# Optimization experiments

Hardware: AMD Instinct MI355X
Metric: run time of the kernel (lower is better)

## Reference

```python
import jax, jax.numpy as jnp
import numpy as np

N, K, D = 65536, 4096, 64


def setup_inputs() -> dict:
    key = jax.random.key(0)
    kx, ke = jax.random.split(key)
    x = jax.random.normal(kx, (N, D), dtype=jnp.float32)
    embed = jax.random.normal(ke, (1, K, D), dtype=jnp.float32)
    return {"x": x, "embed": embed}


def reference(x, embed):
    # Faithful to EuclideanCodebook.forward quantization path:
    #   dist = cdist(flatten, embed, p=2)**2 ; argmin ; one_hot @ embed
    xf = x.astype(jnp.float32)            # [N, D]
    e = embed[0]                          # [K, D]
    # squared euclidean distance via expansion (== cdist(...).pow(2))
    x_sq = jnp.sum(xf * xf, axis=-1, keepdims=True)        # [N, 1]
    e_sq = jnp.sum(e * e, axis=-1)                          # [K]
    dist = jnp.maximum(x_sq + e_sq[None, :] - 2.0 * (xf @ e.T), 0.0)  # [N, K]
    embed_ind = jnp.argmin(dist, axis=-1)                   # [N]
    # one_hot @ embed is exactly a row gather of the codebook
    quantize = e[embed_ind]                                 # [N, D]
    return quantize, embed_ind[None, :]                     # embed_ind kept as [1, N] like torch
```

## Files before the change

kernel.cpp:

```cpp
#include <hip/hip_runtime.h>
#include <math.h>

#define N_ROWS 65536
#define K_CODES 4096
#define NTILES_TOTAL (K_CODES / 32)
#define K_CHUNKS 4
#define NTILES (NTILES_TOTAL / K_CHUNKS)
#define DIM 64
#define NBUF 2
#define ACC_MARGIN 0.005f

typedef __attribute__((ext_vector_type(8))) short bf16x8;
typedef __attribute__((ext_vector_type(4))) float f32x4;

__device__ inline unsigned short f2bf_rne(float f) {
    unsigned u = __float_as_uint(f);
    return (unsigned short)((u + 0x7FFFu + ((u >> 16) & 1u)) >> 16);
}
__device__ inline float bf2f(unsigned short s) {
    return __uint_as_float(((unsigned)s) << 16);
}

__global__ __launch_bounds__(256) void pack_e(const float* __restrict__ embed,
                                              short* __restrict__ e_pk,
                                              float* __restrict__ esq,
                                              float* __restrict__ esqn,
                                              int* __restrict__ count) {
    __shared__ float lds_f[2048];
    const int tile = blockIdx.x;
    const int t = threadIdx.x;
    if (tile == 0 && t == 0) *count = 0;
    const float4* src = (const float4*)(embed + (size_t)tile * 2048);
    ((float4*)lds_f)[t] = src[t];
    ((float4*)lds_f)[t + 256] = src[t + 256];
    __syncthreads();
    const int l = t & 63;
    const int kh = (t >> 6) & 1;
    const int ch = (t >> 7) & 1;
    const int base = (ch * 16 + (l & 15)) * 64 + kh * 32 + ((l >> 4) & 3) * 8;
    bf16x8 vh, vl;
#pragma unroll
    for (int j = 0; j < 8; ++j) {
        float v = lds_f[base + j];
        unsigned short h = f2bf_rne(v);
        vh[j] = (short)h;
        vl[j] = (short)f2bf_rne(v - bf2f(h));
    }
    *(bf16x8*)(e_pk + (size_t)tile * 4096 + t * 8) = vh;
    *(bf16x8*)(e_pk + (size_t)tile * 4096 + 2048 + t * 8) = vl;
    if (t < 32) {
        float s = 0.f;
#pragma unroll
        for (int d = 0; d < 64; ++d) { float v = lds_f[t * 64 + d]; s = fmaf(v, v, s); }
        esq[tile * 32 + t] = s;
        esqn[tile * 32 + t] = -0.5f * s;
    }
}

__global__ __launch_bounds__(256, 4) void vq_main(const float* __restrict__ x,
                                                  const short* __restrict__ e_pk,
                                                  const float* __restrict__ esqn,
                                                  float* __restrict__ b1s,
                                                  float* __restrict__ b2s,
                                                  int* __restrict__ i1s) {
    __shared__ __align__(16) char lds[NBUF][8192];
    __shared__ __align__(16) float lds_q[NBUF][64];
    const int tid = threadIdx.x;
    const int wid = tid >> 6;
    const int l = tid & 63;
    const int c16 = l & 15;
    const int rgrp = (l >> 4) & 3;
    const int kc = blockIdx.x & (K_CHUNKS - 1);
    const int rg = blockIdx.x >> 2;
    const int rowbase = rg * 128 + wid * 32;
    const int tile0 = kc * NTILES;

    bf16x8 ah[2][2], al[2][2];
#pragma unroll
    for (int rh = 0; rh < 2; ++rh) {
        const float* xr = x + (size_t)(rowbase + rh * 16 + c16) * DIM;
#pragma unroll
        for (int kh = 0; kh < 2; ++kh) {
            const float* p = xr + kh * 32 + rgrp * 8;
#pragma unroll
            for (int j = 0; j < 8; ++j) {
                float v = p[j];
                unsigned short h = f2bf_rne(v);
                ah[rh][kh][j] = (short)h;
                al[rh][kh][j] = (short)f2bf_rne(v - bf2f(h));
            }
        }
    }

    float b1[8], b2[8];
    int i1[8];
#pragma unroll
    for (int i = 0; i < 8; ++i) { b1[i] = -3.0e38f; b2[i] = -3.0e38f; i1[i] = 0; }

    auto stage = [&](int t, int b) {
        const char* gsrc = (const char*)e_pk + (size_t)(tile0 + t) * 8192 + tid * 16;
        __builtin_amdgcn_global_load_lds(
            (const __attribute__((address_space(1))) void*)gsrc,
            (__attribute__((address_space(3))) void*)(&lds[b][wid * 1024]), 16, 0, 0);
        __builtin_amdgcn_global_load_lds(
            (const __attribute__((address_space(1))) void*)(gsrc + 4096),
            (__attribute__((address_space(3))) void*)(&lds[b][4096 + wid * 1024]), 16, 0, 0);
        const float* qsrc = esqn + (size_t)(tile0 + t) * 32 + l;
        __builtin_amdgcn_global_load_lds(
            (const __attribute__((address_space(1))) void*)qsrc,
            (__attribute__((address_space(3))) void*)(&lds_q[b][0]), 4, 0, 0);
    };

    stage(0, 0);

    for (int t = 0; t < NTILES; ++t) {
        const int cur = t & 1;
        asm volatile("s_waitcnt vmcnt(0) lgkmcnt(0)" ::: "memory");
        __builtin_amdgcn_sched_barrier(0);
        __builtin_amdgcn_s_barrier();
        __builtin_amdgcn_sched_barrier(0);
        if (t + 1 < NTILES) stage(t + 1, cur ^ 1);

        const float eq0 = lds_q[cur][c16];
        const float eq1 = lds_q[cur][16 + c16];
        const int ci0 = (tile0 + t) * 32 + c16;
        const int ci1 = ci0 + 16;

        bf16x8 bh[2][2], bl[2][2];
#pragma unroll
        for (int ch = 0; ch < 2; ++ch)
#pragma unroll
            for (int kh = 0; kh < 2; ++kh) {
                const int fo = ((ch * 2 + kh) * 64 + l) * 16;
                bh[ch][kh] = *(const bf16x8*)(&lds[cur][fo]);
                bl[ch][kh] = *(const bf16x8*)(&lds[cur][4096 + fo]);
            }

        f32x4 a00 = {eq0, eq0, eq0, eq0};
        f32x4 a01 = {eq1, eq1, eq1, eq1};
        f32x4 a10 = {eq0, eq0, eq0, eq0};
        f32x4 a11 = {eq1, eq1, eq1, eq1};

        __builtin_amdgcn_s_setprio(1);
#pragma unroll
        for (int kh = 0; kh < 2; ++kh) {
            a00 = __builtin_amdgcn_mfma_f32_16x16x32_bf16(ah[0][kh], bh[0][kh], a00, 0, 0, 0);
            a01 = __builtin_amdgcn_mfma_f32_16x16x32_bf16(ah[0][kh], bh[1][kh], a01, 0, 0, 0);
            a10 = __builtin_amdgcn_mfma_f32_16x16x32_bf16(ah[1][kh], bh[0][kh], a10, 0, 0, 0);
            a11 = __builtin_amdgcn_mfma_f32_16x16x32_bf16(ah[1][kh], bh[1][kh], a11, 0, 0, 0);
            a00 = __builtin_amdgcn_mfma_f32_16x16x32_bf16(ah[0][kh], bl[0][kh], a00, 0, 0, 0);
            a01 = __builtin_amdgcn_mfma_f32_16x16x32_bf16(ah[0][kh], bl[1][kh], a01, 0, 0, 0);
            a10 = __builtin_amdgcn_mfma_f32_16x16x32_bf16(ah[1][kh], bl[0][kh], a10, 0, 0, 0);
            a11 = __builtin_amdgcn_mfma_f32_16x16x32_bf16(ah[1][kh], bl[1][kh], a11, 0, 0, 0);
            a00 = __builtin_amdgcn_mfma_f32_16x16x32_bf16(al[0][kh], bh[0][kh], a00, 0, 0, 0);
            a01 = __builtin_amdgcn_mfma_f32_16x16x32_bf16(al[0][kh], bh[1][kh], a01, 0, 0, 0);
            a10 = __builtin_amdgcn_mfma_f32_16x16x32_bf16(al[1][kh], bh[0][kh], a10, 0, 0, 0);
            a11 = __builtin_amdgcn_mfma_f32_16x16x32_bf16(al[1][kh], bh[1][kh], a11, 0, 0, 0);
        }
        __builtin_amdgcn_s_setprio(0);

#define TRACK2(V0, V1, E)                                            \
        {                                                            \
            float v0 = (V0), v1 = (V1);                              \
            bool g0 = v0 > b1[E];                                    \
            b2[E] = __builtin_amdgcn_fmed3f(v0, b1[E], b2[E]);       \
            b1[E] = fmaxf(v0, b1[E]);                                \
            i1[E] = g0 ? ci0 : i1[E];                                \
            bool g1 = v1 > b1[E];                                    \
            b2[E] = __builtin_amdgcn_fmed3f(v1, b1[E], b2[E]);       \
            b1[E] = fmaxf(v1, b1[E]);                                \
            i1[E] = g1 ? ci1 : i1[E];                                \
        }
#pragma unroll
        for (int j = 0; j < 4; ++j) {
            TRACK2(a00[j], a01[j], j)
            TRACK2(a10[j], a11[j], 4 + j)
        }
#undef TRACK2
    }

#pragma unroll
    for (int e = 0; e < 8; ++e) {
#pragma unroll
        for (int m = 1; m <= 8; m <<= 1) {
            float ob1 = __shfl_xor(b1[e], m);
            float ob2 = __shfl_xor(b2[e], m);
            int oi = __shfl_xor(i1[e], m);
            float nb2 = fmaxf(fminf(b1[e], ob1), fmaxf(b2[e], ob2));
            bool take = ob1 > b1[e];
            b1[e] = take ? ob1 : b1[e];
            i1[e] = take ? oi : i1[e];
            b2[e] = nb2;
        }
        if (c16 == 0) {
            int row = rowbase + (e >> 2) * 16 + rgrp * 4 + (e & 3);
            b1s[(size_t)kc * N_ROWS + row] = b1[e];
            b2s[(size_t)kc * N_ROWS + row] = b2[e];
            i1s[(size_t)kc * N_ROWS + row] = i1[e];
        }
    }
}

__global__ __launch_bounds__(256) void vq_merge_gather(const float* __restrict__ embed,
                                                       const float* __restrict__ b1s,
                                                       const float* __restrict__ b2s,
                                                       const int* __restrict__ i1s,
                                                       float* __restrict__ out_q,
                                                       float* __restrict__ out_ind,
                                                       int* __restrict__ list,
                                                       int* __restrict__ count) {
    int t = blockIdx.x * 256 + threadIdx.x;
    int r = t >> 3, q = t & 7;
    float m1 = b1s[r];
    float m2 = b2s[r];
    int idx = i1s[r];
#pragma unroll
    for (int c = 1; c < K_CHUNKS; ++c) {
        float c1 = b1s[(size_t)c * N_ROWS + r];
        float c2 = b2s[(size_t)c * N_ROWS + r];
        int ci = i1s[(size_t)c * N_ROWS + r];
        bool take = c1 > m1;
        m2 = fmaxf(fminf(m1, c1), fmaxf(m2, c2));
        m1 = fmaxf(m1, c1);
        idx = take ? ci : idx;
    }
    const float4* src = (const float4*)(embed + (size_t)idx * DIM + q * 8);
    float4* dst = (float4*)(out_q + (size_t)r * DIM + q * 8);
    dst[0] = src[0];
    dst[1] = src[1];
    if (q == 0) {
        out_ind[r] = (float)idx;
        if (m1 - m2 < ACC_MARGIN) {
            int p = atomicAdd(count, 1);
            list[p] = r;
        }
    }
}

__global__ __launch_bounds__(256) void vq_rescore(const float* __restrict__ x,
                                                  const float* __restrict__ embed,
                                                  const float* __restrict__ esq,
                                                  const int* __restrict__ list,
                                                  const int* __restrict__ count,
                                                  float* __restrict__ out_q,
                                                  float* __restrict__ out_ind) {
    __shared__ float xs[64];
    __shared__ float sk[256];
    __shared__ int si[256];
    const int tid = threadIdx.x;
    const int n = *count;
    for (int f = blockIdx.x; f < n; f += gridDim.x) {
        const int row = list[f];
        if (tid < 16) ((float4*)xs)[tid] = ((const float4*)(x + (size_t)row * DIM))[tid];
        __syncthreads();
        float best = 3.0e38f;
        int bi = 0;
        for (int i = 0; i < 16; ++i) {
            int c = tid + (i << 8);
            const float* e = embed + (size_t)c * DIM;
            float d0 = 0, d1 = 0, d2 = 0, d3 = 0;
#pragma unroll
            for (int d = 0; d < 64; d += 4) {
                d0 = fmaf(xs[d + 0], e[d + 0], d0);
                d1 = fmaf(xs[d + 1], e[d + 1], d1);
                d2 = fmaf(xs[d + 2], e[d + 2], d2);
                d3 = fmaf(xs[d + 3], e[d + 3], d3);
            }
            float key = fmaf(-2.f, (d0 + d1) + (d2 + d3), esq[c]);
            if (key < best) { best = key; bi = c; }
        }
        sk[tid] = best; si[tid] = bi;
        __syncthreads();
        for (int s = 128; s > 0; s >>= 1) {
            if (tid < s) {
                float ok = sk[tid + s]; int oi = si[tid + s];
                if (ok < sk[tid] || (ok == sk[tid] && oi < si[tid])) { sk[tid] = ok; si[tid] = oi; }
            }
            __syncthreads();
        }
        if (tid == 0) out_ind[row] = (float)si[0];
        if (tid < 16) {
            const float4* src = (const float4*)(embed + (size_t)si[0] * DIM);
            ((float4*)(out_q + (size_t)row * DIM))[tid] = src[tid];
        }
        __syncthreads();
    }
}

extern "C" void kernel_launch(void* const* d_in, const int* in_sizes, int n_in,
                              void* d_out, int out_size, void* d_ws, size_t ws_size,
                              hipStream_t stream) {
    const float* x = (const float*)d_in[0];
    const float* embed = (const float*)d_in[1];
    float* out = (float*)d_out;
    float* out_ind = out + (size_t)N_ROWS * DIM;

    char* ws = (char*)d_ws;
    short* e_pk = (short*)ws;
    size_t off = 1 << 20;
    float* esq = (float*)(ws + off);  off += 17 << 10;
    float* esqn = (float*)(ws + off); off += 17 << 10;
    float* b1s = (float*)(ws + off);  off += (size_t)K_CHUNKS * N_ROWS * 4;
    float* b2s = (float*)(ws + off);  off += (size_t)K_CHUNKS * N_ROWS * 4;
    int* i1s = (int*)(ws + off);      off += (size_t)K_CHUNKS * N_ROWS * 4;
    int* list = (int*)(ws + off);     off += (size_t)N_ROWS * 4;
    int* count = (int*)(ws + off);

    pack_e<<<NTILES_TOTAL, 256, 0, stream>>>(embed, e_pk, esq, esqn, count);
    vq_main<<<(N_ROWS / 128) * K_CHUNKS, 256, 0, stream>>>(x, e_pk, esqn, b1s, b2s, i1s);
    vq_merge_gather<<<N_ROWS * 8 / 256, 256, 0, stream>>>(embed, b1s, b2s, i1s,
                                                          out, out_ind, list, count);
    vq_rescore<<<512, 256, 0, stream>>>(x, embed, esq, list, count, out, out_ind);
}
```

Before: 149.7 us.

## Software-pipeline MFMA tiles with deferred argmin tracking across two accumulator sets

Unrolls the tile loop by two and keeps two sets of accumulators, so the argmin/top-2 tracking for one tile is issued after the MFMAs for the next tile, overlapping VALU compare work with matrix-core latency. B fragments are now loaded from LDS inside the kh loop rather than all up front. Launch bounds drop from 4 to 2 waves-per-EU minimum to allow the extra accumulator registers, which may reduce occupancy.

Result: no change. 151.5 us (+1.2%).

```diff
diff --git a/kernel.cpp b/kernel.cpp
--- a/kernel.cpp
+++ b/kernel.cpp
@@ -57,7 +57,7 @@
     }
 }
 
-__global__ __launch_bounds__(256, 4) void vq_main(const float* __restrict__ x,
+__global__ __launch_bounds__(256, 2) void vq_main(const float* __restrict__ x,
                                                   const short* __restrict__ e_pk,
                                                   const float* __restrict__ esqn,
                                                   float* __restrict__ b1s,
@@ -113,71 +113,90 @@
 
     stage(0, 0);
 
-    for (int t = 0; t < NTILES; ++t) {
-        const int cur = t & 1;
-        asm volatile("s_waitcnt vmcnt(0) lgkmcnt(0)" ::: "memory");
-        __builtin_amdgcn_sched_barrier(0);
-        __builtin_amdgcn_s_barrier();
-        __builtin_amdgcn_sched_barrier(0);
-        if (t + 1 < NTILES) stage(t + 1, cur ^ 1);
-
-        const float eq0 = lds_q[cur][c16];
-        const float eq1 = lds_q[cur][16 + c16];
-        const int ci0 = (tile0 + t) * 32 + c16;
-        const int ci1 = ci0 + 16;
-
-        bf16x8 bh[2][2], bl[2][2];
-#pragma unroll
-        for (int ch = 0; ch < 2; ++ch)
-#pragma unroll
-            for (int kh = 0; kh < 2; ++kh) {
-                const int fo = ((ch * 2 + kh) * 64 + l) * 16;
-                bh[ch][kh] = *(const bf16x8*)(&lds[cur][fo]);
-                bl[ch][kh] = *(const bf16x8*)(&lds[cur][4096 + fo]);
-            }
-
-        f32x4 a00 = {eq0, eq0, eq0, eq0};
-        f32x4 a01 = {eq1, eq1, eq1, eq1};
-        f32x4 a10 = {eq0, eq0, eq0, eq0};
-        f32x4 a11 = {eq1, eq1, eq1, eq1};
-
-        __builtin_amdgcn_s_setprio(1);
-#pragma unroll
-        for (int kh = 0; kh < 2; ++kh) {
-            a00 = __builtin_amdgcn_mfma_f32_16x16x32_bf16(ah[0][kh], bh[0][kh], a00, 0, 0, 0);
-            a01 = __builtin_amdgcn_mfma_f32_16x16x32_bf16(ah[0][kh], bh[1][kh], a01, 0, 0, 0);
-            a10 = __builtin_amdgcn_mfma_f32_16x16x32_bf16(ah[1][kh], bh[0][kh], a10, 0, 0, 0);
-            a11 = __builtin_amdgcn_mfma_f32_16x16x32_bf16(ah[1][kh], bh[1][kh], a11, 0, 0, 0);
-            a00 = __builtin_amdgcn_mfma_f32_16x16x32_bf16(ah[0][kh], bl[0][kh], a00, 0, 0, 0);
-            a01 = __builtin_amdgcn_mfma_f32_16x16x32_bf16(ah[0][kh], bl[1][kh], a01, 0, 0, 0);
-            a10 = __builtin_amdgcn_mfma_f32_16x16x32_bf16(ah[1][kh], bl[0][kh], a10, 0, 0, 0);
-            a11 = __builtin_amdgcn_mfma_f32_16x16x32_bf16(ah[1][kh], bl[1][kh], a11, 0, 0, 0);
-            a00 = __builtin_amdgcn_mfma_f32_16x16x32_bf16(al[0][kh], bh[0][kh], a00, 0, 0, 0);
-            a01 = __builtin_amdgcn_mfma_f32_16x16x32_bf16(al[0][kh], bh[1][kh], a01, 0, 0, 0);
-            a10 = __builtin_amdgcn_mfma_f32_16x16x32_bf16(al[1][kh], bh[0][kh], a10, 0, 0, 0);
-            a11 = __builtin_amdgcn_mfma_f32_16x16x32_bf16(al[1][kh], bh[1][kh], a11, 0, 0, 0);
-        }
-        __builtin_amdgcn_s_setprio(0);
-
-#define TRACK2(V0, V1, E)                                            \
+    f32x4 aA00, aA01, aA10, aA11;
+    f32x4 aB00, aB01, aB10, aB11;
+    int pci0 = 0;
+
+#define BARRIER_STAGE(T, CUR)                                          \
+    asm volatile("s_waitcnt vmcnt(0) lgkmcnt(0)" ::: "memory");        \
+    __builtin_amdgcn_sched_barrier(0);                                 \
+    __builtin_amdgcn_s_barrier();                                      \
+    __builtin_amdgcn_sched_barrier(0);                                 \
+    if ((T) + 1 < NTILES) stage((T) + 1, (CUR) ^ 1);
+
+#define MFMA_TILE(CUR, A00, A01, A10, A11)                             \
+    {                                                                  \
+        const float eq0 = lds_q[CUR][c16];                             \
+        const float eq1 = lds_q[CUR][16 + c16];                        \
+        A00 = (f32x4){eq0, eq0, eq0, eq0};                             \
+        A01 = (f32x4){eq1, eq1, eq1, eq1};                             \
+        A10 = (f32x4){eq0, eq0, eq0, eq0};                             \
+        A11 = (f32x4){eq1, eq1, eq1, eq1};                             \
+        __builtin_amdgcn_s_setprio(1);                                 \
+        _Pragma("unroll")                                              \
+        for (int kh = 0; kh < 2; ++kh) {                               \
+            const int fo0 = ((0 * 2 + kh) * 64 + l) * 16;              \
+            const int fo1 = ((1 * 2 + kh) * 64 + l) * 16;              \
+            const bf16x8 bh0 = *(const bf16x8*)(&lds[CUR][fo0]);       \
+            const bf16x8 bh1 = *(const bf16x8*)(&lds[CUR][fo1]);       \
+            const bf16x8 bl0 = *(const bf16x8*)(&lds[CUR][4096 + fo0]); \
+            const bf16x8 bl1 = *(const bf16x8*)(&lds[CUR][4096 + fo1]); \
+            A00 = __builtin_amdgcn_mfma_f32_16x16x32_bf16(ah[0][kh], bh0, A00, 0, 0, 0); \
+            A01 = __builtin_amdgcn_mfma_f32_16x16x32_bf16(ah[0][kh], bh1, A01, 0, 0, 0); \
+            A10 = __builtin_amdgcn_mfma_f32_16x16x32_bf16(ah[1][kh], bh0, A10, 0, 0, 0); \
+            A11 = __builtin_amdgcn_mfma_f32_16x16x32_bf16(ah[1][kh], bh1, A11, 0, 0, 0); \
+            A00 = __builtin_amdgcn_mfma_f32_16x16x32_bf16(ah[0][kh], bl0, A00, 0, 0, 0); \
+            A01 = __builtin_amdgcn_mfma_f32_16x16x32_bf16(ah[0][kh], bl1, A01, 0, 0, 0); \
+            A10 = __builtin_amdgcn_mfma_f32_16x16x32_bf16(ah[1][kh], bl0, A10, 0, 0, 0); \
+            A11 = __builtin_amdgcn_mfma_f32_16x16x32_bf16(ah[1][kh], bl1, A11, 0, 0, 0); \
+            A00 = __builtin_amdgcn_mfma_f32_16x16x32_bf16(al[0][kh], bh0, A00, 0, 0, 0); \
+            A01 = __builtin_amdgcn_mfma_f32_16x16x32_bf16(al[0][kh], bh1, A01, 0, 0, 0); \
+            A10 = __builtin_amdgcn_mfma_f32_16x16x32_bf16(al[1][kh], bh0, A10, 0, 0, 0); \
+            A11 = __builtin_amdgcn_mfma_f32_16x16x32_bf16(al[1][kh], bh1, A11, 0, 0, 0); \
+        }                                                              \
+        __builtin_amdgcn_s_setprio(0);                                 \
+    }
+
+#define TRACK2(V0, V1, E, CI0, CI1)                                  \
         {                                                            \
             float v0 = (V0), v1 = (V1);                              \
             bool g0 = v0 > b1[E];                                    \
             b2[E] = __builtin_amdgcn_fmed3f(v0, b1[E], b2[E]);       \
             b1[E] = fmaxf(v0, b1[E]);                                \
-            i1[E] = g0 ? ci0 : i1[E];                                \
+            i1[E] = g0 ? (CI0) : i1[E];                              \
             bool g1 = v1 > b1[E];                                    \
             b2[E] = __builtin_amdgcn_fmed3f(v1, b1[E], b2[E]);       \
             b1[E] = fmaxf(v1, b1[E]);                                \
-            i1[E] = g1 ? ci1 : i1[E];                                \
-        }
-#pragma unroll
-        for (int j = 0; j < 4; ++j) {
-            TRACK2(a00[j], a01[j], j)
-            TRACK2(a10[j], a11[j], 4 + j)
-        }
+            i1[E] = g1 ? (CI1) : i1[E];                              \
+        }
+
+#define TRACK_SET(A00, A01, A10, A11, CI0)                             \
+    {                                                                  \
+        const int tci0 = (CI0);                                        \
+        const int tci1 = tci0 + 16;                                    \
+        _Pragma("unroll")                                              \
+        for (int j = 0; j < 4; ++j) {                                  \
+            TRACK2(A00[j], A01[j], j, tci0, tci1)                      \
+            TRACK2(A10[j], A11[j], 4 + j, tci0, tci1)                  \
+        }                                                              \
+    }
+
+#pragma unroll 1
+    for (int t = 0; t < NTILES; t += 2) {
+        BARRIER_STAGE(t, 0);
+        MFMA_TILE(0, aA00, aA01, aA10, aA11);
+        if (t > 0) TRACK_SET(aB00, aB01, aB10, aB11, pci0);
+        BARRIER_STAGE(t + 1, 1);
+        MFMA_TILE(1, aB00, aB01, aB10, aB11);
+        TRACK_SET(aA00, aA01, aA10, aA11, (tile0 + t) * 32 + c16);
+        pci0 = (tile0 + t + 1) * 32 + c16;
+    }
+    TRACK_SET(aB00, aB01, aB10, aB11, pci0);
+
+#undef TRACK_SET
 #undef TRACK2
-    }
+#undef MFMA_TILE
+#undef BARRIER_STAGE
 
 #pragma unroll
     for (int e = 0; e < 8; ++e) {
```

## Drop low-bf16 x term in MFMA scoring and batch rescore over rows

Applied to the files above, without the earlier changes.

The main distance kernel stops splitting x into high and low bf16 parts, which removes a third of the MFMA work per tile. The near-tie margin is widened so that more rows fall back to exact fp32 rescoring, which offsets the lost precision. The rescore kernel now handles 8 rows per block and reuses each codebook load across them, and it launches with a larger grid. The risk is that the candidate list grows much longer, so rescore cost could eat the savings, and correctness depends on the margin covering the bf16 error.

Measured after the change: 430.5 us. 188% more time.

```diff
diff --git a/kernel.cpp b/kernel.cpp
--- a/kernel.cpp
+++ b/kernel.cpp
@@ -8,7 +8,8 @@
 #define NTILES (NTILES_TOTAL / K_CHUNKS)
 #define DIM 64
 #define NBUF 2
-#define ACC_MARGIN 0.005f
+#define ACC_MARGIN 0.15f
+#define RR 8
 
 typedef __attribute__((ext_vector_type(8))) short bf16x8;
 typedef __attribute__((ext_vector_type(4))) float f32x4;
@@ -75,7 +76,7 @@
     const int rowbase = rg * 128 + wid * 32;
     const int tile0 = kc * NTILES;
 
-    bf16x8 ah[2][2], al[2][2];
+    bf16x8 ah[2][2];
 #pragma unroll
     for (int rh = 0; rh < 2; ++rh) {
         const float* xr = x + (size_t)(rowbase + rh * 16 + c16) * DIM;
@@ -83,12 +84,8 @@
         for (int kh = 0; kh < 2; ++kh) {
             const float* p = xr + kh * 32 + rgrp * 8;
 #pragma unroll
-            for (int j = 0; j < 8; ++j) {
-                float v = p[j];
-                unsigned short h = f2bf_rne(v);
-                ah[rh][kh][j] = (short)h;
-                al[rh][kh][j] = (short)f2bf_rne(v - bf2f(h));
-            }
+            for (int j = 0; j < 8; ++j)
+                ah[rh][kh][j] = (short)f2bf_rne(p[j]);
         }
     }
 
@@ -152,10 +149,6 @@
             a01 = __builtin_amdgcn_mfma_f32_16x16x32_bf16(ah[0][kh], bl[1][kh], a01, 0, 0, 0);
             a10 = __builtin_amdgcn_mfma_f32_16x16x32_bf16(ah[1][kh], bl[0][kh], a10, 0, 0, 0);
             a11 = __builtin_amdgcn_mfma_f32_16x16x32_bf16(ah[1][kh], bl[1][kh], a11, 0, 0, 0);
-            a00 = __builtin_amdgcn_mfma_f32_16x16x32_bf16(al[0][kh], bh[0][kh], a00, 0, 0, 0);
-            a01 = __builtin_amdgcn_mfma_f32_16x16x32_bf16(al[0][kh], bh[1][kh], a01, 0, 0, 0);
-            a10 = __builtin_amdgcn_mfma_f32_16x16x32_bf16(al[1][kh], bh[0][kh], a10, 0, 0, 0);
-            a11 = __builtin_amdgcn_mfma_f32_16x16x32_bf16(al[1][kh], bh[1][kh], a11, 0, 0, 0);
         }
         __builtin_amdgcn_s_setprio(0);
 
@@ -244,46 +237,72 @@
                                                   const int* __restrict__ count,
                                                   float* __restrict__ out_q,
                                                   float* __restrict__ out_ind) {
-    __shared__ float xs[64];
+    __shared__ float xs[RR][64];
+    __shared__ int rowids[RR];
     __shared__ float sk[256];
     __shared__ int si[256];
     const int tid = threadIdx.x;
     const int n = *count;
-    for (int f = blockIdx.x; f < n; f += gridDim.x) {
-        const int row = list[f];
-        if (tid < 16) ((float4*)xs)[tid] = ((const float4*)(x + (size_t)row * DIM))[tid];
+    for (int base = blockIdx.x * RR; base < n; base += gridDim.x * RR) {
+        const int nr = min(RR, n - base);
         __syncthreads();
-        float best = 3.0e38f;
-        int bi = 0;
+        if (tid < nr) rowids[tid] = list[base + tid];
+        __syncthreads();
+        if (tid < nr * 16) {
+            int r = tid >> 4, q = tid & 15;
+            ((float4*)xs[r])[q] = ((const float4*)(x + (size_t)rowids[r] * DIM))[q];
+        }
+        __syncthreads();
+
+        float best[RR];
+        int bi[RR];
+#pragma unroll
+        for (int r = 0; r < RR; ++r) { best[r] = 3.0e38f; bi[r] = 0; }
+
         for (int i = 0; i < 16; ++i) {
-            int c = tid + (i << 8);
-            const float* e = embed + (size_t)c * DIM;
-            float d0 = 0, d1 = 0, d2 = 0, d3 = 0;
-#pragma unroll
-            for (int d = 0; d < 64; d += 4) {
-                d0 = fmaf(xs[d + 0], e[d + 0], d0);
-                d1 = fmaf(xs[d + 1], e[d + 1], d1);
-                d2 = fmaf(xs[d + 2], e[d + 2], d2);
-                d3 = fmaf(xs[d + 3], e[d + 3], d3);
-            }
-            float key = fmaf(-2.f, (d0 + d1) + (d2 + d3), esq[c]);
-            if (key < best) { best = key; bi = c; }
-        }
-        sk[tid] = best; si[tid] = bi;
-        __syncthreads();
-        for (int s = 128; s > 0; s >>= 1) {
-            if (tid < s) {
-                float ok = sk[tid + s]; int oi = si[tid + s];
-                if (ok < sk[tid] || (ok == sk[tid] && oi < si[tid])) { sk[tid] = ok; si[tid] = oi; }
-            }
+            const int c = tid + (i << 8);
+            const float4* e4 = (const float4*)(embed + (size_t)c * DIM);
+            float dot[RR];
+#pragma unroll
+            for (int r = 0; r < RR; ++r) dot[r] = 0.f;
+#pragma unroll
+            for (int q = 0; q < 16; ++q) {
+                float4 ev = e4[q];
+#pragma unroll
+                for (int r = 0; r < RR; ++r) {
+                    float4 xv = ((const float4*)xs[r])[q];
+                    dot[r] = fmaf(xv.x, ev.x, dot[r]);
+                    dot[r] = fmaf(xv.y, ev.y, dot[r]);
+                    dot[r] = fmaf(xv.z, ev.z, dot[r]);
+                    dot[r] = fmaf(xv.w, ev.w, dot[r]);
+                }
+            }
+            const float eq = esq[c];
+#pragma unroll
+            for (int r = 0; r < RR; ++r) {
+                float key = fmaf(-2.f, dot[r], eq);
+                if (key < best[r]) { best[r] = key; bi[r] = c; }
+            }
+        }
+
+        for (int r = 0; r < nr; ++r) {
+            sk[tid] = best[r];
+            si[tid] = bi[r];
             __syncthreads();
-        }
-        if (tid == 0) out_ind[row] = (float)si[0];
-        if (tid < 16) {
-            const float4* src = (const float4*)(embed + (size_t)si[0] * DIM);
-            ((float4*)(out_q + (size_t)row * DIM))[tid] = src[tid];
-        }
-        __syncthreads();
+            for (int s = 128; s > 0; s >>= 1) {
+                if (tid < s) {
+                    float ok = sk[tid + s]; int oi = si[tid + s];
+                    if (ok < sk[tid] || (ok == sk[tid] && oi < si[tid])) { sk[tid] = ok; si[tid] = oi; }
+                }
+                __syncthreads();
+            }
+            if (tid == 0) out_ind[rowids[r]] = (float)si[0];
+            if (tid < 16) {
+                ((float4*)(out_q + (size_t)rowids[r] * DIM))[tid] =
+                    ((const float4*)(embed + (size_t)si[0] * DIM))[tid];
+            }
+            __syncthreads();
+        }
     }
 }
 
@@ -310,5 +329,5 @@
     vq_main<<<(N_ROWS / 128) * K_CHUNKS, 256, 0, stream>>>(x, e_pk, esqn, b1s, b2s, i1s);
     vq_merge_gather<<<N_ROWS * 8 / 256, 256, 0, stream>>>(embed, b1s, b2s, i1s,
                                                           out, out_ind, list, count);
-    vq_rescore<<<512, 256, 0, stream>>>(x, embed, esq, list, count, out, out_ind);
-}
+    vq_rescore<<<2048, 256, 0, stream>>>(x, embed, esq, list, count, out, out_ind);
+}
```
